# Kernel optimization log

Hardware: AMD Instinct MI355X
Metric: run time of the kernel (lower is better)

The kernel has to match this reference:

```python
import jax, jax.numpy as jnp
import numpy as np

N_NODES = 50000
N_EDGES = 800000
IN_DIM, HID_DIM, NUM_CLASSES = 128, 64, 32
DROP_P = 0.1


def gcn_conv(x, W, b, src, dst, n_nodes):
    """PyG-style GCNConv: x @ W, symmetric normalization with self-loops,
    scatter-add aggregation at dst, then bias. Self-loop contribution is
    added analytically (norm_ii = deg_i^-1) instead of appending edges."""
    h = x @ W  # [N, out]
    deg = jax.ops.segment_sum(jnp.ones((src.shape[0],), h.dtype), dst,
                              num_segments=n_nodes) + 1.0  # +1 for self-loop
    dinv = jax.lax.rsqrt(deg)  # deg >= 1, always finite
    norm = dinv[src] * dinv[dst]  # [E]
    msg = h[src] * norm[:, None]  # gather + scale  [E, out]
    agg = jax.ops.segment_sum(msg, dst, num_segments=n_nodes)
    agg = agg + h * (dinv * dinv)[:, None]  # self-loop term
    return agg + b


def setup_inputs() -> dict:
    key = jax.random.key(0)
    ks = jax.random.split(key, 12)
    x = jax.random.normal(ks[0], (N_NODES, IN_DIM), jnp.float32)
    edge_index = jax.random.randint(ks[1], (2, N_EDGES), 0, N_NODES, jnp.int64)
    # Glorot-ish weights (PyG Linear transform has no bias; bias added post-agg)
    def glorot(k, fan_in, fan_out):
        s = jnp.sqrt(2.0 / (fan_in + fan_out))
        return jax.random.normal(k, (fan_in, fan_out), jnp.float32) * s
    W0 = glorot(ks[2], IN_DIM, HID_DIM)
    b0 = jnp.zeros((HID_DIM,), jnp.float32)
    W1 = glorot(ks[3], HID_DIM, NUM_CLASSES)
    b1 = jnp.zeros((NUM_CLASSES,), jnp.float32)
    W2 = glorot(ks[4], HID_DIM, NUM_CLASSES)
    b2 = jnp.zeros((NUM_CLASSES,), jnp.float32)
    # training-mode randomness, materialized deterministically
    keep = jax.random.bernoulli(ks[5], 1.0 - DROP_P, (N_NODES, HID_DIM))
    dropout_mask = keep.astype(jnp.float32) / (1.0 - DROP_P)
    eps = jax.random.normal(ks[6], (N_NODES, NUM_CLASSES), jnp.float32)
    return {"x": x, "edge_index": edge_index, "W0": W0, "b0": b0,
            "W1": W1, "b1": b1, "W2": W2, "b2": b2,
            "dropout_mask": dropout_mask, "eps": eps}


def reference(x, edge_index, W0, b0, W1, b1, W2, b2, dropout_mask, eps):
    src, dst = edge_index[0], edge_index[1]
    n = x.shape[0]
    h = gcn_conv(x, W0, b0, src, dst, n)
    h = jax.nn.relu(h)
    h = h * dropout_mask  # inverted dropout, training mode
    mu = gcn_conv(h, W1, b1, src, dst, n)
    logvar = gcn_conv(h, W2, b2, src, dst, n)
    # NOTE: source uses std = exp(logvar) (no 0.5 factor)
    z = eps * jnp.exp(logvar) + mu
    return (z, mu, logvar)
```

## Files before the change

kernel.cpp:

```cpp
#include <hip/hip_runtime.h>

#define IN_DIM 128
#define HID 64
#define NC 32
#define SCAN_TILE 2048

__device__ __forceinline__ unsigned short f2bf(float f) {
    unsigned b = __float_as_uint(f);
    unsigned r = (b + 0x7FFFu + ((b >> 16) & 1u)) >> 16;
    return (unsigned short)r;
}
__device__ __forceinline__ float bf2f(unsigned short u) {
    return __uint_as_float(((unsigned)u) << 16);
}

__global__ void hist_kernel(const int* __restrict__ dst, int* __restrict__ deg,
                            int* __restrict__ rank, int E) {
    int e = blockIdx.x * blockDim.x + threadIdx.x;
    if (e < E) rank[e] = atomicAdd(&deg[dst[e]], 1);
}

__global__ __launch_bounds__(256) void scan_tile_kernel(const int* __restrict__ in,
                                                        int* __restrict__ out,
                                                        int* __restrict__ partials, int n) {
    __shared__ int tsum[256];
    int t = threadIdx.x;
    int base = blockIdx.x * SCAN_TILE + t * 8;
    int v[8];
    int s = 0;
    #pragma unroll
    for (int j = 0; j < 8; ++j) {
        int idx = base + j;
        int x = (idx < n) ? in[idx] : 0;
        s += x;
        v[j] = s;
    }
    tsum[t] = s;
    __syncthreads();
    for (int off = 1; off < 256; off <<= 1) {
        int add = (t >= off) ? tsum[t - off] : 0;
        __syncthreads();
        tsum[t] += add;
        __syncthreads();
    }
    int excl = tsum[t] - s;
    #pragma unroll
    for (int j = 0; j < 8; ++j) {
        int idx = base + j;
        if (idx < n) out[idx] = v[j] + excl;
    }
    if (t == 255) partials[blockIdx.x] = tsum[255];
}

__global__ void scan_partials_kernel(int* __restrict__ partials, int nb) {
    if (threadIdx.x == 0 && blockIdx.x == 0) {
        int run = 0;
        for (int b = 0; b < nb; ++b) { int x = partials[b]; partials[b] = run; run += x; }
    }
}

__global__ void rowptr_kernel(const int* __restrict__ scan_buf, const int* __restrict__ partials,
                              int* __restrict__ rowptr, int n) {
    int i = blockIdx.x * blockDim.x + threadIdx.x;
    if (i < n) rowptr[i + 1] = scan_buf[i] + partials[i / SCAN_TILE];
    if (i == 0) rowptr[0] = 0;
}

__global__ void dinv_kernel(const int* __restrict__ deg, float* __restrict__ dinv, int n) {
    int i = blockIdx.x * blockDim.x + threadIdx.x;
    if (i < n) dinv[i] = rsqrtf((float)deg[i] + 1.0f);
}

__global__ void scatter_kernel(const int* __restrict__ src, const int* __restrict__ dst,
                               const int* __restrict__ rank, const int* __restrict__ rowptr,
                               int* __restrict__ e_src, int E) {
    int e = blockIdx.x * blockDim.x + threadIdx.x;
    if (e >= E) return;
    int d = dst[e];
    e_src[rowptr[d] + rank[e]] = src[e];
}

__global__ __launch_bounds__(256) void gemm0_kernel(const float* __restrict__ x,
                                                    const float* __restrict__ W,
                                                    const float* __restrict__ dinv,
                                                    unsigned short* __restrict__ hp0, int n) {
    __shared__ float Ws[IN_DIM * HID];
    __shared__ float xs[16][IN_DIM];
    int tid = threadIdx.x;
    const float4* W4 = (const float4*)W;
    float4* Ws4 = (float4*)Ws;
    #pragma unroll
    for (int j = 0; j < 8; ++j) Ws4[tid + 256 * j] = W4[tid + 256 * j];
    int base = blockIdx.x * 16;
    const float4* x4 = (const float4*)(x + (size_t)base * IN_DIM);
    float4* xs4 = (float4*)xs;
    #pragma unroll
    for (int j = 0; j < 2; ++j) {
        int i = tid + 256 * j;
        if (base + (i >> 5) < n) xs4[i] = x4[i];
    }
    __syncthreads();
    int r = tid >> 4;
    int c4 = (tid & 15) * 4;
    int row = base + r;
    if (row >= n) return;
    float4 acc = make_float4(0.f, 0.f, 0.f, 0.f);
    #pragma unroll
    for (int k = 0; k < IN_DIM; ++k) {
        float xv = xs[r][k];
        float4 w = *(const float4*)&Ws[k * HID + c4];
        acc.x += xv * w.x; acc.y += xv * w.y; acc.z += xv * w.z; acc.w += xv * w.w;
    }
    float dv = dinv[row];
    ushort4 o;
    o.x = f2bf(acc.x * dv); o.y = f2bf(acc.y * dv);
    o.z = f2bf(acc.z * dv); o.w = f2bf(acc.w * dv);
    *(ushort4*)&hp0[(size_t)row * HID + c4] = o;
}

__global__ __launch_bounds__(256) void gather0_kernel(const int* __restrict__ rowptr,
                                                      const int* __restrict__ e_src,
                                                      const unsigned short* __restrict__ hp0,
                                                      const float* __restrict__ dinv,
                                                      const float* __restrict__ b0,
                                                      const float* __restrict__ mask,
                                                      unsigned short* __restrict__ hb, int n) {
    int v = blockIdx.x * 4 + (threadIdx.x >> 6);
    int c = threadIdx.x & 63;
    if (v >= n) return;
    int start = rowptr[v], end = rowptr[v + 1];
    float acc = 0.f;
    for (int p = start; p < end; p += 8) {
        int ss[8];
        #pragma unroll
        for (int i = 0; i < 8; ++i) {
            int q = p + i;
            ss[i] = e_src[q < end ? q : end - 1];
        }
        unsigned short gu[8];
        #pragma unroll
        for (int i = 0; i < 8; ++i) gu[i] = hp0[(size_t)ss[i] * HID + c];
        #pragma unroll
        for (int i = 0; i < 8; ++i) acc += (p + i < end) ? bf2f(gu[i]) : 0.f;
    }
    float dv = dinv[v];
    float selfv = bf2f(hp0[(size_t)v * HID + c]);
    float val = dv * (acc + selfv) + b0[c];
    val = val > 0.f ? val : 0.f;
    val = val * mask[(size_t)v * HID + c] * dv;
    hb[(size_t)v * HID + c] = f2bf(val);
}

__global__ __launch_bounds__(256) void gather2_kernel(const int* __restrict__ rowptr,
                                                      const int* __restrict__ e_src,
                                                      const unsigned short* __restrict__ hb,
                                                      float* __restrict__ T, int n) {
    int v = blockIdx.x * 4 + (threadIdx.x >> 6);
    int c = threadIdx.x & 63;
    if (v >= n) return;
    int start = rowptr[v], end = rowptr[v + 1];
    float acc = 0.f;
    for (int p = start; p < end; p += 8) {
        int ss[8];
        #pragma unroll
        for (int i = 0; i < 8; ++i) {
            int q = p + i;
            ss[i] = e_src[q < end ? q : end - 1];
        }
        unsigned short gu[8];
        #pragma unroll
        for (int i = 0; i < 8; ++i) gu[i] = hb[(size_t)ss[i] * HID + c];
        #pragma unroll
        for (int i = 0; i < 8; ++i) acc += (p + i < end) ? bf2f(gu[i]) : 0.f;
    }
    acc += bf2f(hb[(size_t)v * HID + c]);
    T[(size_t)v * HID + c] = acc;
}

__global__ __launch_bounds__(256) void gemm2_kernel(const float* __restrict__ T,
                                                    const float* __restrict__ dinv,
                                                    const float* __restrict__ W1,
                                                    const float* __restrict__ W2,
                                                    const float* __restrict__ b1,
                                                    const float* __restrict__ b2,
                                                    const float* __restrict__ eps,
                                                    float* __restrict__ zout,
                                                    float* __restrict__ muout,
                                                    float* __restrict__ lvout, int n) {
    __shared__ float W1s[HID * NC];
    __shared__ float W2s[HID * NC];
    __shared__ float Ss[16][HID];
    int tid = threadIdx.x;
    const float4* W14 = (const float4*)W1;
    const float4* W24 = (const float4*)W2;
    float4* W1s4 = (float4*)W1s;
    float4* W2s4 = (float4*)W2s;
    #pragma unroll
    for (int j = 0; j < 2; ++j) {
        W1s4[tid + 256 * j] = W14[tid + 256 * j];
        W2s4[tid + 256 * j] = W24[tid + 256 * j];
    }
    int base = blockIdx.x * 16;
    {
        int row = base + (tid >> 4);
        int cc = (tid & 15) * 4;
        if (row < n) {
            float dv = dinv[row];
            float4 tv = *(const float4*)&T[(size_t)row * HID + cc];
            float4 s;
            s.x = dv * tv.x; s.y = dv * tv.y; s.z = dv * tv.z; s.w = dv * tv.w;
            *(float4*)&Ss[tid >> 4][cc] = s;
        }
    }
    __syncthreads();
    int r = tid >> 4;
    int q = tid & 15;
    int head = q >> 3;
    int c4 = (q & 7) * 4;
    int row = base + r;
    if (row >= n) return;
    const float* Wp = head ? W2s : W1s;
    float4 acc = make_float4(0.f, 0.f, 0.f, 0.f);
    #pragma unroll
    for (int k = 0; k < HID; ++k) {
        float xv = Ss[r][k];
        float4 w = *(const float4*)&Wp[k * NC + c4];
        acc.x += xv * w.x; acc.y += xv * w.y; acc.z += xv * w.z; acc.w += xv * w.w;
    }
    const float* bb = head ? b2 : b1;
    acc.x += bb[c4]; acc.y += bb[c4 + 1]; acc.z += bb[c4 + 2]; acc.w += bb[c4 + 3];
    int lane = threadIdx.x & 63;
    float4 other;
    other.x = __shfl(acc.x, lane ^ 8);
    other.y = __shfl(acc.y, lane ^ 8);
    other.z = __shfl(acc.z, lane ^ 8);
    other.w = __shfl(acc.w, lane ^ 8);
    size_t o = (size_t)row * NC + c4;
    if (head == 0) {
        *(float4*)&muout[o] = acc;
        float4 ev = *(const float4*)&eps[o];
        float4 z;
        z.x = ev.x * expf(other.x) + acc.x;
        z.y = ev.y * expf(other.y) + acc.y;
        z.z = ev.z * expf(other.z) + acc.z;
        z.w = ev.w * expf(other.w) + acc.w;
        *(float4*)&zout[o] = z;
    } else {
        *(float4*)&lvout[o] = acc;
    }
}

extern "C" void kernel_launch(void* const* d_in, const int* in_sizes, int n_in,
                              void* d_out, int out_size, void* d_ws, size_t ws_size,
                              hipStream_t stream) {
    const float* x    = (const float*)d_in[0];
    const int*   ei   = (const int*)d_in[1];
    const float* W0   = (const float*)d_in[2];
    const float* b0   = (const float*)d_in[3];
    const float* W1   = (const float*)d_in[4];
    const float* b1   = (const float*)d_in[5];
    const float* W2   = (const float*)d_in[6];
    const float* b2   = (const float*)d_in[7];
    const float* mask = (const float*)d_in[8];
    const float* eps  = (const float*)d_in[9];

    int n = in_sizes[0] / IN_DIM;
    int E = in_sizes[1] / 2;
    const int* src = ei;
    const int* dst = ei + E;

    int*   ws_i    = (int*)d_ws;
    int*   deg_i   = ws_i;
    int*   rowptr  = deg_i + 50048;
    int*   scanbuf = rowptr + 50056;
    int*   partials= scanbuf + 50048;
    float* dinv    = (float*)(partials + 64);
    int*   rank    = (int*)(dinv + 50048);
    int*   e_src   = rank + E;
    unsigned short* hp0 = (unsigned short*)(e_src + E);
    unsigned short* hb  = hp0 + (size_t)n * HID;
    float* T       = (float*)(hb + (size_t)n * HID);

    float* zout  = (float*)d_out;
    float* muout = zout + (size_t)n * NC;
    float* lvout = muout + (size_t)n * NC;

    int nb = (n + SCAN_TILE - 1) / SCAN_TILE;

    hipMemsetAsync(deg_i, 0, 50048 * sizeof(int), stream);

    hist_kernel<<<(E + 255) / 256, 256, 0, stream>>>(dst, deg_i, rank, E);
    scan_tile_kernel<<<nb, 256, 0, stream>>>(deg_i, scanbuf, partials, n);
    scan_partials_kernel<<<1, 64, 0, stream>>>(partials, nb);
    rowptr_kernel<<<(n + 255) / 256, 256, 0, stream>>>(scanbuf, partials, rowptr, n);
    dinv_kernel<<<(n + 255) / 256, 256, 0, stream>>>(deg_i, dinv, n);
    gemm0_kernel<<<(n + 15) / 16, 256, 0, stream>>>(x, W0, dinv, hp0, n);
    scatter_kernel<<<(E + 255) / 256, 256, 0, stream>>>(src, dst, rank, rowptr, e_src, E);
    gather0_kernel<<<(n + 3) / 4, 256, 0, stream>>>(rowptr, e_src, hp0, dinv, b0, mask, hb, n);
    gather2_kernel<<<(n + 3) / 4, 256, 0, stream>>>(rowptr, e_src, hb, T, n);
    gemm2_kernel<<<(n + 15) / 16, 256, 0, stream>>>(T, dinv, W1, W2, b1, b2, eps,
                                                    zout, muout, lvout, n);
}
```

Baseline: 262.9 us.

## Split gathers into two column-half passes with edge-parallel half-waves

Each gather kernel now runs twice, once per 32-column half of the feature dimension. Within a wavefront the two 32-lane halves take alternating edges and combine their partial sums with a cross-lane shuffle. The aim is to shrink each pass's working set of gathered rows (64 bytes per row instead of 128) so more of it stays in cache, and to double edge-level parallelism per wave. In exchange, the edge indices are read twice, there are extra launches, and half the lanes sit idle in the epilogue. The rowptr and dinv kernels are also fused into one launch.

```diff
diff --git a/kernel.cpp b/kernel.cpp
--- a/kernel.cpp
+++ b/kernel.cpp
@@ -59,16 +59,15 @@
     }
 }
 
-__global__ void rowptr_kernel(const int* __restrict__ scan_buf, const int* __restrict__ partials,
-                              int* __restrict__ rowptr, int n) {
+__global__ void rowptr_dinv_kernel(const int* __restrict__ scan_buf, const int* __restrict__ partials,
+                                   const int* __restrict__ deg, int* __restrict__ rowptr,
+                                   float* __restrict__ dinv, int n) {
     int i = blockIdx.x * blockDim.x + threadIdx.x;
-    if (i < n) rowptr[i + 1] = scan_buf[i] + partials[i / SCAN_TILE];
+    if (i < n) {
+        rowptr[i + 1] = scan_buf[i] + partials[i / SCAN_TILE];
+        dinv[i] = rsqrtf((float)deg[i] + 1.0f);
+    }
     if (i == 0) rowptr[0] = 0;
-}
-
-__global__ void dinv_kernel(const int* __restrict__ deg, float* __restrict__ dinv, int n) {
-    int i = blockIdx.x * blockDim.x + threadIdx.x;
-    if (i < n) dinv[i] = rsqrtf((float)deg[i] + 1.0f);
 }
 
 __global__ void scatter_kernel(const int* __restrict__ src, const int* __restrict__ dst,
@@ -124,57 +123,68 @@
                                                       const float* __restrict__ dinv,
                                                       const float* __restrict__ b0,
                                                       const float* __restrict__ mask,
-                                                      unsigned short* __restrict__ hb, int n) {
+                                                      unsigned short* __restrict__ hb,
+                                                      int n, int colbase) {
     int v = blockIdx.x * 4 + (threadIdx.x >> 6);
-    int c = threadIdx.x & 63;
     if (v >= n) return;
+    int lane = threadIdx.x & 63;
+    int half = lane >> 5;
+    int col = colbase + (lane & 31);
     int start = rowptr[v], end = rowptr[v + 1];
     float acc = 0.f;
-    for (int p = start; p < end; p += 8) {
-        int ss[8];
+    for (int p = start; p < end; p += 16) {
+        int ss[8]; bool vv[8];
         #pragma unroll
         for (int i = 0; i < 8; ++i) {
-            int q = p + i;
-            ss[i] = e_src[q < end ? q : end - 1];
+            int q = p + 2 * i + half;
+            vv[i] = q < end;
+            ss[i] = e_src[vv[i] ? q : end - 1];
         }
         unsigned short gu[8];
         #pragma unroll
-        for (int i = 0; i < 8; ++i) gu[i] = hp0[(size_t)ss[i] * HID + c];
-        #pragma unroll
-        for (int i = 0; i < 8; ++i) acc += (p + i < end) ? bf2f(gu[i]) : 0.f;
-    }
-    float dv = dinv[v];
-    float selfv = bf2f(hp0[(size_t)v * HID + c]);
-    float val = dv * (acc + selfv) + b0[c];
-    val = val > 0.f ? val : 0.f;
-    val = val * mask[(size_t)v * HID + c] * dv;
-    hb[(size_t)v * HID + c] = f2bf(val);
+        for (int i = 0; i < 8; ++i) gu[i] = hp0[(size_t)ss[i] * HID + col];
+        #pragma unroll
+        for (int i = 0; i < 8; ++i) acc += vv[i] ? bf2f(gu[i]) : 0.f;
+    }
+    acc += __shfl(acc, lane ^ 32);
+    if (half == 0) {
+        float dv = dinv[v];
+        float val = dv * (acc + bf2f(hp0[(size_t)v * HID + col])) + b0[col];
+        val = val > 0.f ? val : 0.f;
+        val = val * mask[(size_t)v * HID + col] * dv;
+        hb[(size_t)v * HID + col] = f2bf(val);
+    }
 }
 
 __global__ __launch_bounds__(256) void gather2_kernel(const int* __restrict__ rowptr,
                                                       const int* __restrict__ e_src,
                                                       const unsigned short* __restrict__ hb,
-                                                      float* __restrict__ T, int n) {
+                                                      float* __restrict__ T, int n, int colbase) {
     int v = blockIdx.x * 4 + (threadIdx.x >> 6);
-    int c = threadIdx.x & 63;
     if (v >= n) return;
+    int lane = threadIdx.x & 63;
+    int half = lane >> 5;
+    int col = colbase + (lane & 31);
     int start = rowptr[v], end = rowptr[v + 1];
     float acc = 0.f;
-    for (int p = start; p < end; p += 8) {
-        int ss[8];
+    for (int p = start; p < end; p += 16) {
+        int ss[8]; bool vv[8];
         #pragma unroll
         for (int i = 0; i < 8; ++i) {
-            int q = p + i;
-            ss[i] = e_src[q < end ? q : end - 1];
+            int q = p + 2 * i + half;
+            vv[i] = q < end;
+            ss[i] = e_src[vv[i] ? q : end - 1];
         }
         unsigned short gu[8];
         #pragma unroll
-        for (int i = 0; i < 8; ++i) gu[i] = hb[(size_t)ss[i] * HID + c];
-        #pragma unroll
-        for (int i = 0; i < 8; ++i) acc += (p + i < end) ? bf2f(gu[i]) : 0.f;
-    }
-    acc += bf2f(hb[(size_t)v * HID + c]);
-    T[(size_t)v * HID + c] = acc;
+        for (int i = 0; i < 8; ++i) gu[i] = hb[(size_t)ss[i] * HID + col];
+        #pragma unroll
+        for (int i = 0; i < 8; ++i) acc += vv[i] ? bf2f(gu[i]) : 0.f;
+    }
+    acc += __shfl(acc, lane ^ 32);
+    if (half == 0) {
+        T[(size_t)v * HID + col] = acc + bf2f(hb[(size_t)v * HID + col]);
+    }
 }
 
 __global__ __launch_bounds__(256) void gemm2_kernel(const float* __restrict__ T,
@@ -286,18 +296,21 @@
     float* lvout = muout + (size_t)n * NC;
 
     int nb = (n + SCAN_TILE - 1) / SCAN_TILE;
+    int ngb = (n + 3) / 4;
 
     hipMemsetAsync(deg_i, 0, 50048 * sizeof(int), stream);
 
     hist_kernel<<<(E + 255) / 256, 256, 0, stream>>>(dst, deg_i, rank, E);
     scan_tile_kernel<<<nb, 256, 0, stream>>>(deg_i, scanbuf, partials, n);
     scan_partials_kernel<<<1, 64, 0, stream>>>(partials, nb);
-    rowptr_kernel<<<(n + 255) / 256, 256, 0, stream>>>(scanbuf, partials, rowptr, n);
-    dinv_kernel<<<(n + 255) / 256, 256, 0, stream>>>(deg_i, dinv, n);
+    rowptr_dinv_kernel<<<(n + 255) / 256, 256, 0, stream>>>(scanbuf, partials, deg_i,
+                                                            rowptr, dinv, n);
     gemm0_kernel<<<(n + 15) / 16, 256, 0, stream>>>(x, W0, dinv, hp0, n);
     scatter_kernel<<<(E + 255) / 256, 256, 0, stream>>>(src, dst, rank, rowptr, e_src, E);
-    gather0_kernel<<<(n + 3) / 4, 256, 0, stream>>>(rowptr, e_src, hp0, dinv, b0, mask, hb, n);
-    gather2_kernel<<<(n + 3) / 4, 256, 0, stream>>>(rowptr, e_src, hb, T, n);
+    gather0_kernel<<<ngb, 256, 0, stream>>>(rowptr, e_src, hp0, dinv, b0, mask, hb, n, 0);
+    gather0_kernel<<<ngb, 256, 0, stream>>>(rowptr, e_src, hp0, dinv, b0, mask, hb, n, 32);
+    gather2_kernel<<<ngb, 256, 0, stream>>>(rowptr, e_src, hb, T, n, 0);
+    gather2_kernel<<<ngb, 256, 0, stream>>>(rowptr, e_src, hb, T, n, 32);
     gemm2_kernel<<<(n + 15) / 16, 256, 0, stream>>>(T, dinv, W1, W2, b1, b2, eps,
                                                     zout, muout, lvout, n);
 }
```

Result: slower. 281.7 us (+7.1%).
